# Kernel tuning notes

Hardware: AMD Instinct MI355X
Metric: run time of the kernel (lower is better)

## Reference

```python
import jax, jax.numpy as jnp
import numpy as np

H = 12        # num attention heads
W = 256       # one-sided window (attention_window // 2)
NEG = -1e9    # additive mask value


def setup_inputs() -> dict:
    key = jax.random.key(0)
    ks = jax.random.split(key, 6)
    B, S, D = 2, 4096, 768
    inp = {
        "hidden_states": jax.random.normal(ks[0], (B, S, D), dtype=jnp.float32),
        "attention_mask": jnp.zeros((B, S), dtype=jnp.float32),
        "Wq": jax.random.normal(ks[1], (D, D), dtype=jnp.float32) * 0.02,
        "bq": jnp.zeros((D,), dtype=jnp.float32),
        "Wk": jax.random.normal(ks[2], (D, D), dtype=jnp.float32) * 0.02,
        "bk": jnp.zeros((D,), dtype=jnp.float32),
        "Wv": jax.random.normal(ks[3], (D, D), dtype=jnp.float32) * 0.02,
        "bv": jnp.zeros((D,), dtype=jnp.float32),
        "Wo": jax.random.normal(ks[4], (D, D), dtype=jnp.float32) * 0.02,
        "bo": jnp.zeros((D,), dtype=jnp.float32),
    }
    return inp


def _sliding_window_attn(hidden_states, attention_mask, Wq, bq, Wk, bk, Wv, bv, Wo, bo):
    B, S, D = hidden_states.shape
    dh = D // H
    b = W                 # chunk size == one-sided window
    nb = S // b           # number of chunks (S must be multiple of W)

    # projections; Longformer scales the query by 1/sqrt(d_head)
    q = (hidden_states @ Wq.T + bq) / jnp.sqrt(jnp.float32(dh))
    k = hidden_states @ Wk.T + bk
    v = hidden_states @ Wv.T + bv

    # [B, H, S, dh]
    q = q.reshape(B, S, H, dh).transpose(0, 2, 1, 3)
    k = k.reshape(B, S, H, dh).transpose(0, 2, 1, 3)
    v = v.reshape(B, S, H, dh).transpose(0, 2, 1, 3)

    # chunk queries: [B, H, nb, b, dh]
    qb = q.reshape(B, H, nb, b, dh)

    # pad K/V by one chunk on each side, gather 3 consecutive chunks per query chunk
    kp = jnp.pad(k, ((0, 0), (0, 0), (b, b), (0, 0)))
    vp = jnp.pad(v, ((0, 0), (0, 0), (b, b), (0, 0)))
    idx = jnp.arange(nb)[:, None] * b + jnp.arange(3 * b)[None, :]  # [nb, 3b] into padded seq
    kw = kp[:, :, idx]  # [B, H, nb, 3b, dh]
    vw = vp[:, :, idx]  # [B, H, nb, 3b, dh]

    # banded scores: [B, H, nb, b, 3b]
    scores = jnp.einsum("bhnqd,bhnkd->bhnqk", qb, kw)

    # band mask: query at local pos qi (global n*b+qi) vs key at local pos ki
    # (global n*b + ki - b); relative offset = ki - b - qi, keep |offset| <= W
    rel = jnp.arange(3 * b)[None, :] - b - jnp.arange(b)[:, None]      # [b, 3b]
    band = jnp.abs(rel) <= W
    # sequence-boundary mask: key global position must lie in [0, S)
    kpos = idx - b                                                      # [nb, 3b]
    inbounds = (kpos >= 0) & (kpos < S)
    valid = band[None, :, :] & inbounds[:, None, :]                     # [nb, b, 3b]

    # key padding bias from attention_mask (wrapper passes attention_mask * -1)
    neg_mask = attention_mask * -1.0                                    # [B, S]
    mp = jnp.pad(neg_mask, ((0, 0), (b, b)))
    key_bias = mp[:, idx]                                               # [B, nb, 3b]

    scores = scores + key_bias[:, None, :, None, :]
    scores = jnp.where(valid[None, None], scores, NEG)

    probs = jax.nn.softmax(scores, axis=-1)
    ctx = jnp.einsum("bhnqk,bhnkd->bhnqd", probs, vw)                   # [B, H, nb, b, dh]
    ctx = ctx.reshape(B, H, S, dh).transpose(0, 2, 1, 3).reshape(B, S, D)

    return ctx @ Wo.T + bo


def reference(hidden_states, attention_mask, Wq, bq, Wk, bk, Wv, bv, Wo, bo):
    return _sliding_window_attn(hidden_states, attention_mask,
                                Wq, bq, Wk, bk, Wv, bv, Wo, bo)
```

## Files before the change

### kernel.cpp

```cpp
#include <hip/hip_runtime.h>
#include <hip/hip_bf16.h>
#include <stdint.h>

#define NH 12
#define DH 64
#define SEQ 4096
#define DM 768
#define NEGV -1e9f
#define LOG2E 1.4426950408889634f
#define QSCALE 0.1803368801111601f

using bf16x8 = __attribute__((ext_vector_type(8))) short;
using f32x4  = __attribute__((ext_vector_type(4))) float;

static __device__ __forceinline__ short f2bf(float f) {
  unsigned u = __builtin_bit_cast(unsigned, f);
  u += 0x7fffu + ((u >> 16) & 1u);
  return (short)(u >> 16);
}

static __device__ __forceinline__ unsigned pack2bf(float lo, float hi) {
  unsigned a = __builtin_bit_cast(unsigned, lo);
  a += 0x7fffu + ((a >> 16) & 1u);
  unsigned b = __builtin_bit_cast(unsigned, hi);
  b += 0x7fffu + ((b >> 16) & 1u);
  return (a >> 16) | (b & 0xffff0000u);
}

static __device__ __forceinline__ void gload16(const void* g, void* l) {
  __builtin_amdgcn_global_load_lds(
      (const __attribute__((address_space(1))) unsigned*)g,
      (__attribute__((address_space(3))) unsigned*)l, 16, 0, 0);
}

static __device__ __forceinline__ f32x4 mfma16(bf16x8 a, bf16x8 b, f32x4 c) {
  return __builtin_amdgcn_mfma_f32_16x16x32_bf16(a, b, c, 0, 0, 0);
}

#define SBAR() __builtin_amdgcn_sched_barrier(0)
#define WAIT8() asm volatile("s_waitcnt vmcnt(8)" ::: "memory")
#define WAIT4() asm volatile("s_waitcnt vmcnt(4)" ::: "memory")
#define WAIT0() asm volatile("s_waitcnt vmcnt(0)" ::: "memory")
#define LKWAIT() asm volatile("s_waitcnt lgkmcnt(0)" ::: "memory")
#define HBAR() __builtin_amdgcn_s_barrier()

__global__ __launch_bounds__(256) void cvt_x(const float* __restrict__ X,
                                             short* __restrict__ Xb, int n4) {
  int i = blockIdx.x * 256 + threadIdx.x;
  if (i >= n4) return;
  float4 v = ((const float4*)X)[i];
  short4 o; o.x = f2bf(v.x); o.y = f2bf(v.y); o.z = f2bf(v.z); o.w = f2bf(v.w);
  ((short4*)Xb)[i] = o;
}

__global__ __launch_bounds__(256) void cvt_w(
    const float* __restrict__ Wq, const float* __restrict__ Wk,
    const float* __restrict__ Wv, const float* __restrict__ Wo,
    short* __restrict__ Wqkv, short* __restrict__ Wob) {
  int i = blockIdx.x * 256 + threadIdx.x;
  const int n1 = 2304 * 768 / 4;
  if (i < n1) {
    int e = i * 4;
    int row = e / 768;
    const float* src;
    float sc = 1.0f;
    if (row < 768)       { src = Wq + e; sc = QSCALE; }
    else if (row < 1536) { src = Wk + e - 768 * 768; }
    else                 { src = Wv + e - 1536 * 768; }
    float4 v = *(const float4*)src;
    short4 o; o.x = f2bf(v.x * sc); o.y = f2bf(v.y * sc);
    o.z = f2bf(v.z * sc); o.w = f2bf(v.w * sc);
    ((short4*)Wqkv)[i] = o;
  } else {
    int j = i - n1;
    if (j >= 768 * 768 / 4) return;
    float4 v = ((const float4*)Wo)[j];
    short4 o; o.x = f2bf(v.x); o.y = f2bf(v.y); o.z = f2bf(v.z); o.w = f2bf(v.w);
    ((short4*)Wob)[j] = o;
  }
}

#define GEMM_PIPELINE(SM, AG, BG, ACC, LANE, WR, WC)                           \
  {                                                                            \
    const int l15 = (LANE) & 15, gw = (LANE) >> 4;                             \
    const int s_ = (l15 >> 1) & 3;                                             \
    const int fcol = ((gw ^ s_) << 3);                                         \
    const int NT = 24;                                             \
    auto stage = [&](int t) {                                                  \
      short* ab = (SM) + ((t & 3) << 12);                                      \
      short* bb = (SM) + 16384 + ((t & 3) << 12);                              \
      int kt = t << 5;                                                         \
      gload16((AG) + kt, ab + ldst);                                           \
      gload16((AG) + kt + 64 * 768, ab + ldst + 2048);                         \
      gload16((BG) + kt, bb + ldst);                                           \
      gload16((BG) + kt + 64 * 768, bb + ldst + 2048);                         \
    };                                                                         \
    auto compute = [&](int t) {                                                \
      const short* ab = (SM) + ((t & 3) << 12);                                \
      const short* bb = (SM) + 16384 + ((t & 3) << 12);                        \
      bf16x8 af[4], bf[4];                                                     \
      _Pragma("unroll") for (int mi = 0; mi < 4; ++mi)                         \
          af[mi] = *(const bf16x8*)(ab + ((WR) + mi * 16 + l15) * 32 + fcol);  \
      _Pragma("unroll") for (int ni = 0; ni < 4; ++ni)                         \
          bf[ni] = *(const bf16x8*)(bb + ((WC) + ni * 16 + l15) * 32 + fcol);  \
      __builtin_amdgcn_s_setprio(1);                                           \
      _Pragma("unroll") for (int mi = 0; mi < 4; ++mi)                         \
          _Pragma("unroll") for (int ni = 0; ni < 4; ++ni)                     \
              ACC[mi][ni] = mfma16(af[mi], bf[ni], ACC[mi][ni]);               \
      __builtin_amdgcn_s_setprio(0);                                           \
    };                                                                         \
    stage(0); stage(1); stage(2);                                              \
    SBAR();                                                                    \
    _Pragma("unroll 1") for (int i = 0; i < NT - 3; ++i) {                     \
      SBAR(); WAIT8(); HBAR(); SBAR();                                         \
      stage(i + 3);                                                            \
      SBAR();                                                                  \
      compute(i);                                                              \
    }                                                                          \
    SBAR(); WAIT8(); HBAR(); SBAR(); compute(NT - 3);                          \
    SBAR(); WAIT4(); HBAR(); SBAR(); compute(NT - 2);                          \
    SBAR(); WAIT0(); HBAR(); SBAR(); compute(NT - 1);                          \
  }

__global__ __launch_bounds__(256) void gemm_qkv(
    const short* __restrict__ Xb, const short* __restrict__ Wqkv,
    const float* __restrict__ bq, const float* __restrict__ bk,
    const float* __restrict__ bv,
    short* __restrict__ qO, short* __restrict__ kO, short* __restrict__ vT) {
  __shared__ __align__(16) short sm[32768];
  const int tid = threadIdx.x, lane = tid & 63, wid = tid >> 6;
  const int xcd = blockIdx.x & 7, kk = blockIdx.x >> 3;
  const int m0 = (xcd * 8 + (kk & 7)) * 128;
  const int n0 = (kk >> 3) * 128;
  const int wr = (wid >> 1) * 64, wc = (wid & 1) * 64;
  const int srow = tid >> 2;
  const int scol = (((tid & 3) ^ ((srow >> 1) & 3)) << 3);
  const short* Ag = Xb + (m0 + srow) * 768 + scol;
  const short* Bg = Wqkv + (n0 + srow) * 768 + scol;
  const int ldst = tid * 8;

  const int src = n0 / 768;
  const int nloc = n0 % 768;
  float bias[4];
#pragma unroll
  for (int ni = 0; ni < 4; ++ni) {
    int c = nloc + wc + ni * 16 + (lane & 15);
    bias[ni] = (src == 0) ? bq[c] * QSCALE : (src == 1) ? bk[c] : bv[c];
  }
  WAIT0(); SBAR();

  f32x4 acc[4][4] = {};
  GEMM_PIPELINE(sm, Ag, Bg, acc, lane, wr, wc);

  const int bb = m0 >> 12;
  const int s0 = m0 & (SEQ - 1);
  __syncthreads();
  if (src < 2) {
#pragma unroll
    for (int mi = 0; mi < 4; ++mi)
#pragma unroll
      for (int ni = 0; ni < 4; ++ni) {
        int row = wr + mi * 16 + ((lane >> 4) << 2);
        int col = wc + ni * 16 + (lane & 15);
#pragma unroll
        for (int r = 0; r < 4; ++r)
          sm[(row + r) * 132 + col] = f2bf(acc[mi][ni][r] + bias[ni]);
      }
    __syncthreads();
    short* dst = (src == 0) ? qO : kO;
    for (int u = tid; u < 8192; u += 256) {
      int r = u >> 6, cp = (u & 63) << 1;
      unsigned val = *(const unsigned*)&sm[r * 132 + cp];
      int c = nloc + cp;
      int h = c >> 6, d = c & 63;
      *(unsigned*)&dst[(((bb * NH + h) * SEQ) + s0 + r) * DH + d] = val;
    }
  } else {
#pragma unroll
    for (int mi = 0; mi < 4; ++mi)
#pragma unroll
      for (int ni = 0; ni < 4; ++ni) {
        int row = wr + mi * 16 + ((lane >> 4) << 2);
        int col = wc + ni * 16 + (lane & 15);
        short4 pk;
        pk.x = f2bf(acc[mi][ni][0] + bias[ni]);
        pk.y = f2bf(acc[mi][ni][1] + bias[ni]);
        pk.z = f2bf(acc[mi][ni][2] + bias[ni]);
        pk.w = f2bf(acc[mi][ni][3] + bias[ni]);
        *(short4*)&sm[col * 132 + row] = pk;
      }
    __syncthreads();
    for (int u = tid; u < 8192; u += 256) {
      int cc = u >> 6, rp = (u & 63) << 1;
      unsigned val = *(const unsigned*)&sm[cc * 132 + rp];
      int c = nloc + cc;
      int h = c >> 6, d = c & 63;
      *(unsigned*)&vT[(((bb * NH + h) * DH) + d) * SEQ + s0 + rp] = val;
    }
  }
}

__global__ __launch_bounds__(512, 4) void attn(
    const short* __restrict__ qI, const short* __restrict__ kI,
    const short* __restrict__ vT, const float* __restrict__ amask,
    short* __restrict__ ctx) {
  __shared__ __align__(16) short Ks[128 * 64];
  __shared__ __align__(16) short Vs[64 * 128];
  __shared__ __align__(16) short Ps[8][16 * 132];
  __shared__ __align__(16) float BiasL[768];
  const int tid = threadIdx.x, lane = tid & 63, wid = tid >> 6;
  const int vb_id = (blockIdx.x & 7) * 96 + (blockIdx.x >> 3);
  const int strip = vb_id & 31;
  const int hh = (vb_id >> 5) % 12;
  const int bb = vb_id / 384;
  const int s0 = strip * 128;
  const int n = s0 >> 8;
  const int i0 = s0 & 255;
  const int base = (n - 1) * 256;
  const int bh = bb * NH + hh;
  const int m = lane & 15, hq = lane >> 4;
  const int swz = m & 7;
  const int iw = i0 + (wid << 4);

  const short* qbase = qI + ((size_t)(bh * SEQ) + s0 + (wid << 4)) * DH;
  const bf16x8 aq0 = *(const bf16x8*)(qbase + m * DH + (hq << 3));
  const bf16x8 aq1 = *(const bf16x8*)(qbase + m * DH + 32 + (hq << 3));

  const int kb_s0 = m * 64 + ((hq ^ swz) << 3);
  const int kb_s1 = m * 64 + (((hq + 4) ^ swz) << 3);
  const int vk0 = m * 128 + ((hq ^ swz) << 3);
  const int vk1 = m * 128 + (((hq + 4) ^ swz) << 3);
  const int vk2 = m * 128 + (((hq + 8) ^ swz) << 3);
  const int vk3 = m * 128 + (((hq + 12) ^ swz) << 3);
  short* Pw = Ps[wid];
  const int pwr = m * 132;

  const int e0 = tid * 8, e1 = tid * 8 + 4096;
  const int kj0 = e0 >> 6, kj1 = e1 >> 6;
  const int ksrc0 = kj0 * DH + ((((e0 >> 3) & 7) ^ (kj0 & 7)) << 3);
  const int ksrc1 = kj1 * DH + ((((e1 >> 3) & 7) ^ (kj1 & 7)) << 3);
  const int vd0 = e0 >> 7, vd1 = e1 >> 7;
  const int vsrc0 = vd0 * SEQ + ((((e0 >> 3) & 15) ^ (vd0 & 7)) << 3);
  const int vsrc1 = vd1 * SEQ + ((((e1 >> 3) & 15) ^ (vd1 & 7)) << 3);

  const short* kg0 = kI + (size_t)bh * SEQ * DH;
  const short* vg0 = vT + (size_t)bh * DH * SEQ;

  if (tid < 192) {
    int idx = base + tid * 4;
    idx = idx < 0 ? 0 : (idx > SEQ - 4 ? SEQ - 4 : idx);
    float4 bv = *(const float4*)(amask + bb * SEQ + idx);
    *(float4*)&BiasL[tid * 4] = bv;
  }

  int cl0 = (n == 0) ? 2 : 0;
  if (i0 == 128 && cl0 < 1) cl0 = 1;
  int chi = (i0 == 0) ? 4 : 5;
  if (n == 15) chi = 3;

  uint4 rk0, rk1, rv0, rv1;
  {
    const int kpos0 = base + (cl0 << 7);
    const short* kb = kg0 + (size_t)kpos0 * DH;
    rk0 = *(const uint4*)(kb + ksrc0);
    rk1 = *(const uint4*)(kb + ksrc1);
    const short* vbp = vg0 + kpos0;
    rv0 = *(const uint4*)(vbp + vsrc0);
    rv1 = *(const uint4*)(vbp + vsrc1);
  }

  f32x4 acc[4] = {};
  float mrow = -1e30f, lrow = 0.f;

#pragma unroll 1
  for (int cc = cl0; cc <= chi; ++cc) {
    const int j0 = cc << 7;
    SBAR(); LKWAIT(); HBAR(); SBAR();
    *(uint4*)((short*)Ks + e0) = rk0;
    *(uint4*)((short*)Ks + e1) = rk1;
    *(uint4*)((short*)Vs + e0) = rv0;
    *(uint4*)((short*)Vs + e1) = rv1;
    SBAR(); LKWAIT(); HBAR(); SBAR();

    f32x4 sc[8];
    __builtin_amdgcn_s_setprio(1);
#pragma unroll
    for (int jt = 0; jt < 8; ++jt) {
      bf16x8 k0 = *(const bf16x8*)(Ks + jt * 1024 + kb_s0);
      bf16x8 k1 = *(const bf16x8*)(Ks + jt * 1024 + kb_s1);
      f32x4 z = {};
      z = mfma16(k0, aq0, z);
      z = mfma16(k1, aq1, z);
      sc[jt] = z;
    }
    __builtin_amdgcn_s_setprio(0);

    if (cc < chi) {
      const int kposn = base + ((cc + 1) << 7);
      const short* kb = kg0 + (size_t)kposn * DH;
      rk0 = *(const uint4*)(kb + ksrc0);
      rk1 = *(const uint4*)(kb + ksrc1);
      const short* vbp = vg0 + kposn;
      rv0 = *(const uint4*)(vbp + vsrc0);
      rv1 = *(const uint4*)(vbp + vsrc1);
    }

    float mn = mrow;
    const bool interior = (j0 >= iw + 15) && (j0 <= iw + 385);
    const float* bl = BiasL + j0 + (hq << 2);
    if (interior) {
#pragma unroll
      for (int jt = 0; jt < 8; ++jt) {
        float4 b4 = *(const float4*)(bl + jt * 16);
#pragma unroll
        for (int r = 0; r < 4; ++r) {
          float s = fmaf(-LOG2E, (&b4.x)[r], sc[jt][r]);
          sc[jt][r] = s;
          mn = fmaxf(mn, s);
        }
      }
    } else {
      const int iq = iw + m;
#pragma unroll
      for (int jt = 0; jt < 8; ++jt) {
        float4 b4 = *(const float4*)(bl + jt * 16);
        const int jb = j0 + jt * 16 + (hq << 2);
#pragma unroll
        for (int r = 0; r < 4; ++r) {
          int j = jb + r;
          float s = fmaf(-LOG2E, (&b4.x)[r], sc[jt][r]);
          s = (j >= iq && j <= iq + 512) ? s : NEGV;
          sc[jt][r] = s;
          mn = fmaxf(mn, s);
        }
      }
    }
    mn = fmaxf(mn, __shfl_xor(mn, 16));
    mn = fmaxf(mn, __shfl_xor(mn, 32));

    const bool resc = !__all(mn - mrow <= 4.0f);
    const float mbase = resc ? mn : mrow;

    float l0 = 0.f;
#pragma unroll
    for (int jt = 0; jt < 8; ++jt) {
      float p0 = exp2f(sc[jt][0] - mbase);
      float p1 = exp2f(sc[jt][1] - mbase);
      float p2 = exp2f(sc[jt][2] - mbase);
      float p3 = exp2f(sc[jt][3] - mbase);
      l0 += (p0 + p1) + (p2 + p3);
      uint2 u;
      u.x = pack2bf(p0, p1);
      u.y = pack2bf(p2, p3);
      *(uint2*)(Pw + pwr + jt * 16 + (hq << 2)) = u;
    }
    l0 += __shfl_xor(l0, 16);
    l0 += __shfl_xor(l0, 32);
    if (resc) {
      const float scl = exp2f(mrow - mn);
      lrow = lrow * scl + l0;
      mrow = mn;
      const float s0r = __shfl(scl, (hq << 2) + 0);
      const float s1r = __shfl(scl, (hq << 2) + 1);
      const float s2r = __shfl(scl, (hq << 2) + 2);
      const float s3r = __shfl(scl, (hq << 2) + 3);
#pragma unroll
      for (int nt = 0; nt < 4; ++nt) {
        acc[nt][0] *= s0r; acc[nt][1] *= s1r;
        acc[nt][2] *= s2r; acc[nt][3] *= s3r;
      }
    } else {
      lrow += l0;
    }

    LKWAIT(); SBAR();

    __builtin_amdgcn_s_setprio(1);
#pragma unroll
    for (int ks = 0; ks < 4; ++ks) {
      bf16x8 pa = *(const bf16x8*)(Pw + pwr + ks * 32 + (hq << 3));
      const int vkk = (ks == 0) ? vk0 : (ks == 1) ? vk1 : (ks == 2) ? vk2 : vk3;
#pragma unroll
      for (int nt = 0; nt < 4; ++nt) {
        bf16x8 vv = *(const bf16x8*)(Vs + nt * 2048 + vkk);
        acc[nt] = mfma16(pa, vv, acc[nt]);
      }
    }
    __builtin_amdgcn_s_setprio(0);
  }

  const float inv = 1.0f / lrow;
  const float i0r = __shfl(inv, (hq << 2) + 0);
  const float i1r = __shfl(inv, (hq << 2) + 1);
  const float i2r = __shfl(inv, (hq << 2) + 2);
  const float i3r = __shfl(inv, (hq << 2) + 3);
#pragma unroll
  for (int nt = 0; nt < 4; ++nt) {
    Pw[((hq << 2) + 0) * 72 + nt * 16 + m] = f2bf(acc[nt][0] * i0r);
    Pw[((hq << 2) + 1) * 72 + nt * 16 + m] = f2bf(acc[nt][1] * i1r);
    Pw[((hq << 2) + 2) * 72 + nt * 16 + m] = f2bf(acc[nt][2] * i2r);
    Pw[((hq << 2) + 3) * 72 + nt * 16 + m] = f2bf(acc[nt][3] * i3r);
  }
  LKWAIT(); SBAR();
#pragma unroll
  for (int it = 0; it < 2; ++it) {
    int row = it * 8 + (lane >> 3);
    bf16x8 val = *(const bf16x8*)(Pw + row * 72 + ((lane & 7) << 3));
    *(bf16x8*)(ctx + ((size_t)(bb * SEQ) + s0 + (wid << 4) + row) * DM +
               hh * DH + ((lane & 7) << 3)) = val;
  }
}

__global__ __launch_bounds__(256) void gemm_out(
    const short* __restrict__ Cb, const short* __restrict__ Wob,
    const float* __restrict__ bo, float* __restrict__ out) {
  __shared__ __align__(16) short sm[32768];
  const int tid = threadIdx.x, lane = tid & 63, wid = tid >> 6;
  const int xcd = blockIdx.x & 7, kk = blockIdx.x >> 3;
  const int m0 = (xcd * 8 + (kk & 7)) * 128;
  const int n0 = (kk >> 3) * 128;
  const int wr = (wid >> 1) * 64, wc = (wid & 1) * 64;
  const int srow = tid >> 2;
  const int scol = (((tid & 3) ^ ((srow >> 1) & 3)) << 3);
  const short* Ag = Cb + (m0 + srow) * 768 + scol;
  const short* Bg = Wob + (n0 + srow) * 768 + scol;
  const int ldst = tid * 8;

  float bias[4];
#pragma unroll
  for (int ni = 0; ni < 4; ++ni)
    bias[ni] = bo[n0 + wc + ni * 16 + (lane & 15)];
  WAIT0(); SBAR();

  f32x4 acc[4][4] = {};
  GEMM_PIPELINE(sm, Ag, Bg, acc, lane, wr, wc);

#pragma unroll
  for (int mi = 0; mi < 4; ++mi)
#pragma unroll
    for (int ni = 0; ni < 4; ++ni) {
      int row = m0 + wr + mi * 16 + ((lane >> 4) << 2);
      int col = n0 + wc + ni * 16 + (lane & 15);
#pragma unroll
      for (int r = 0; r < 4; ++r)
        out[(row + r) * DM + col] = acc[mi][ni][r] + bias[ni];
    }
}

extern "C" void kernel_launch(void* const* d_in, const int* in_sizes, int n_in,
                              void* d_out, int out_size, void* d_ws, size_t ws_size,
                              hipStream_t stream) {
  (void)in_sizes; (void)n_in; (void)out_size; (void)ws_size;
  const float* hs    = (const float*)d_in[0];
  const float* amask = (const float*)d_in[1];
  const float* Wq = (const float*)d_in[2];
  const float* bq = (const float*)d_in[3];
  const float* Wk = (const float*)d_in[4];
  const float* bk = (const float*)d_in[5];
  const float* Wv = (const float*)d_in[6];
  const float* bv = (const float*)d_in[7];
  const float* Wo = (const float*)d_in[8];
  const float* bo = (const float*)d_in[9];
  float* out = (float*)d_out;
  char* ws = (char*)d_ws;
  short* Xb   = (short*)(ws);
  short* Wqkv = (short*)(ws + 12582912);
  short* Wob  = (short*)(ws + 16121856);
  short* qB   = (short*)(ws + 17301504);
  short* kB   = (short*)(ws + 29884416);
  short* vTB  = (short*)(ws + 42467328);
  short* ctx  = Xb;

  cvt_x<<<dim3(6144), dim3(256), 0, stream>>>(hs, Xb, 8192 * 768 / 4);
  cvt_w<<<dim3(2304), dim3(256), 0, stream>>>(Wq, Wk, Wv, Wo, Wqkv, Wob);
  gemm_qkv<<<dim3(1152), dim3(256), 0, stream>>>(Xb, Wqkv, bq, bk, bv, qB, kB, vTB);
  attn<<<dim3(768), dim3(512), 0, stream>>>(qB, kB, vTB, amask, ctx);
  gemm_out<<<dim3(384), dim3(256), 0, stream>>>(ctx, Wob, bo, out);
}
```

Before: 145.0 us.

## Double-buffer K/V tiles in LDS with direct global-to-LDS async loads

Replaces the register-staged K/V prefetch (global→registers→LDS writes) with direct global-to-LDS loads into a double-buffered shared-memory ring. The next chunk is issued into the alternate buffer at the top of each iteration, so the load overlaps the QK and PV MFMA work. This drops the per-iteration register round-trip and LDS store phase and frees VGPRs. In exchange it doubles K/V LDS usage and removes the occupancy hint from launch_bounds, which may reduce blocks per CU.

```diff
diff --git a/kernel.cpp b/kernel.cpp
--- a/kernel.cpp
+++ b/kernel.cpp
@@ -200,12 +200,12 @@
   }
 }
 
-__global__ __launch_bounds__(512, 4) void attn(
+__global__ __launch_bounds__(512) void attn(
     const short* __restrict__ qI, const short* __restrict__ kI,
     const short* __restrict__ vT, const float* __restrict__ amask,
     short* __restrict__ ctx) {
-  __shared__ __align__(16) short Ks[128 * 64];
-  __shared__ __align__(16) short Vs[64 * 128];
+  __shared__ __align__(16) short Ks[2][8192];
+  __shared__ __align__(16) short Vs[2][8192];
   __shared__ __align__(16) short Ps[8][16 * 132];
   __shared__ __align__(16) float BiasL[768];
   const int tid = threadIdx.x, lane = tid & 63, wid = tid >> 6;
@@ -258,52 +258,43 @@
   int chi = (i0 == 0) ? 4 : 5;
   if (n == 15) chi = 3;
 
-  uint4 rk0, rk1, rv0, rv1;
-  {
-    const int kpos0 = base + (cl0 << 7);
+  auto stageKV = [&](int c, int buf) {
+    const int kpos0 = base + (c << 7);
     const short* kb = kg0 + (size_t)kpos0 * DH;
-    rk0 = *(const uint4*)(kb + ksrc0);
-    rk1 = *(const uint4*)(kb + ksrc1);
+    gload16(kb + ksrc0, (short*)Ks[buf] + e0);
+    gload16(kb + ksrc1, (short*)Ks[buf] + e1);
     const short* vbp = vg0 + kpos0;
-    rv0 = *(const uint4*)(vbp + vsrc0);
-    rv1 = *(const uint4*)(vbp + vsrc1);
-  }
+    gload16(vbp + vsrc0, (short*)Vs[buf] + e0);
+    gload16(vbp + vsrc1, (short*)Vs[buf] + e1);
+  };
+
+  stageKV(cl0, 0);
 
   f32x4 acc[4] = {};
   float mrow = -1e30f, lrow = 0.f;
+  int p = 0;
 
 #pragma unroll 1
   for (int cc = cl0; cc <= chi; ++cc) {
     const int j0 = cc << 7;
-    SBAR(); LKWAIT(); HBAR(); SBAR();
-    *(uint4*)((short*)Ks + e0) = rk0;
-    *(uint4*)((short*)Ks + e1) = rk1;
-    *(uint4*)((short*)Vs + e0) = rv0;
-    *(uint4*)((short*)Vs + e1) = rv1;
-    SBAR(); LKWAIT(); HBAR(); SBAR();
-
+    SBAR(); WAIT0(); HBAR(); SBAR();
+    if (cc < chi) stageKV(cc + 1, p ^ 1);
+    SBAR();
+
+    const short* Kp = Ks[p];
+    const short* Vp = Vs[p];
     f32x4 sc[8];
     __builtin_amdgcn_s_setprio(1);
 #pragma unroll
     for (int jt = 0; jt < 8; ++jt) {
-      bf16x8 k0 = *(const bf16x8*)(Ks + jt * 1024 + kb_s0);
-      bf16x8 k1 = *(const bf16x8*)(Ks + jt * 1024 + kb_s1);
+      bf16x8 k0 = *(const bf16x8*)(Kp + jt * 1024 + kb_s0);
+      bf16x8 k1 = *(const bf16x8*)(Kp + jt * 1024 + kb_s1);
       f32x4 z = {};
       z = mfma16(k0, aq0, z);
       z = mfma16(k1, aq1, z);
       sc[jt] = z;
     }
     __builtin_amdgcn_s_setprio(0);
-
-    if (cc < chi) {
-      const int kposn = base + ((cc + 1) << 7);
-      const short* kb = kg0 + (size_t)kposn * DH;
-      rk0 = *(const uint4*)(kb + ksrc0);
-      rk1 = *(const uint4*)(kb + ksrc1);
-      const short* vbp = vg0 + kposn;
-      rv0 = *(const uint4*)(vbp + vsrc0);
-      rv1 = *(const uint4*)(vbp + vsrc1);
-    }
 
     float mn = mrow;
     const bool interior = (j0 >= iw + 15) && (j0 <= iw + 385);
@@ -382,11 +373,12 @@
       const int vkk = (ks == 0) ? vk0 : (ks == 1) ? vk1 : (ks == 2) ? vk2 : vk3;
 #pragma unroll
       for (int nt = 0; nt < 4; ++nt) {
-        bf16x8 vv = *(const bf16x8*)(Vs + nt * 2048 + vkk);
+        bf16x8 vv = *(const bf16x8*)(Vp + nt * 2048 + vkk);
         acc[nt] = mfma16(pa, vv, acc[nt]);
       }
     }
     __builtin_amdgcn_s_setprio(0);
+    p ^= 1;
   }
 
   const float inv = 1.0f / lrow;
```

Result: faster. 135.9 us (-6.3%).

## Process two query tiles per wave in attention with 4-wave blocks and direct LDS loads

Applied to the files above, without the earlier changes.

The attention kernel now runs 4 waves per block, with each wave handling 32 query rows as two 16-row MFMA tiles. Each K and V fragment read from LDS therefore feeds twice as many MFMAs. The register-staged K/V prefetch is replaced by gload16 direct-to-LDS loads between plain barriers, which drops the overlap with compute. The softmax now uses per-lane partial maxima with a lazy rescale threshold of 8, defers the row-sum reduction to the end, and folds -log2e into the mask bias. Register pressure rises from the doubled accumulators, and removing the prefetch may expose load latency.

```diff
diff --git a/kernel.cpp b/kernel.cpp
--- a/kernel.cpp
+++ b/kernel.cpp
@@ -200,13 +200,13 @@
   }
 }
 
-__global__ __launch_bounds__(512, 4) void attn(
+__global__ __launch_bounds__(256) void attn(
     const short* __restrict__ qI, const short* __restrict__ kI,
     const short* __restrict__ vT, const float* __restrict__ amask,
     short* __restrict__ ctx) {
-  __shared__ __align__(16) short Ks[128 * 64];
-  __shared__ __align__(16) short Vs[64 * 128];
-  __shared__ __align__(16) short Ps[8][16 * 132];
+  __shared__ __align__(16) short Ks[8192];
+  __shared__ __align__(16) short Vs[8192];
+  __shared__ __align__(16) short Ps[4][32 * 132];
   __shared__ __align__(16) float BiasL[768];
   const int tid = threadIdx.x, lane = tid & 63, wid = tid >> 6;
   const int vb_id = (blockIdx.x & 7) * 96 + (blockIdx.x >> 3);
@@ -220,11 +220,13 @@
   const int bh = bb * NH + hh;
   const int m = lane & 15, hq = lane >> 4;
   const int swz = m & 7;
-  const int iw = i0 + (wid << 4);
-
-  const short* qbase = qI + ((size_t)(bh * SEQ) + s0 + (wid << 4)) * DH;
-  const bf16x8 aq0 = *(const bf16x8*)(qbase + m * DH + (hq << 3));
-  const bf16x8 aq1 = *(const bf16x8*)(qbase + m * DH + 32 + (hq << 3));
+  const int iw = i0 + (wid << 5);
+
+  const short* qbase = qI + ((size_t)(bh * SEQ) + s0 + (wid << 5)) * DH;
+  bf16x8 aq00 = *(const bf16x8*)(qbase + m * DH + (hq << 3));
+  bf16x8 aq01 = *(const bf16x8*)(qbase + m * DH + 32 + (hq << 3));
+  bf16x8 aq10 = *(const bf16x8*)(qbase + (16 + m) * DH + (hq << 3));
+  bf16x8 aq11 = *(const bf16x8*)(qbase + (16 + m) * DH + 32 + (hq << 3));
 
   const int kb_s0 = m * 64 + ((hq ^ swz) << 3);
   const int kb_s1 = m * 64 + (((hq + 4) ^ swz) << 3);
@@ -233,15 +235,18 @@
   const int vk2 = m * 128 + (((hq + 8) ^ swz) << 3);
   const int vk3 = m * 128 + (((hq + 12) ^ swz) << 3);
   short* Pw = Ps[wid];
-  const int pwr = m * 132;
-
-  const int e0 = tid * 8, e1 = tid * 8 + 4096;
-  const int kj0 = e0 >> 6, kj1 = e1 >> 6;
-  const int ksrc0 = kj0 * DH + ((((e0 >> 3) & 7) ^ (kj0 & 7)) << 3);
-  const int ksrc1 = kj1 * DH + ((((e1 >> 3) & 7) ^ (kj1 & 7)) << 3);
-  const int vd0 = e0 >> 7, vd1 = e1 >> 7;
-  const int vsrc0 = vd0 * SEQ + ((((e0 >> 3) & 15) ^ (vd0 & 7)) << 3);
-  const int vsrc1 = vd1 * SEQ + ((((e1 >> 3) & 15) ^ (vd1 & 7)) << 3);
+  const int pwr0 = m * 132;
+  const int pwr1 = (16 + m) * 132;
+
+  int ksrcA[1], dummy;
+  (void)dummy; (void)ksrcA;
+  const int eb = tid * 8;
+#define KSRC(p) ({ int e_ = (p)*2048 + eb; int kj_ = e_ >> 6;                 \
+                   kj_ * DH + ((((e_ >> 3) & 7) ^ (kj_ & 7)) << 3); })
+#define VSRC(p) ({ int e_ = (p)*2048 + eb; int vd_ = e_ >> 7;                 \
+                   vd_ * SEQ + ((((e_ >> 3) & 15) ^ (vd_ & 7)) << 3); })
+  const int ks0 = KSRC(0), ks1 = KSRC(1), ks2 = KSRC(2), ks3 = KSRC(3);
+  const int vs0 = VSRC(0), vs1 = VSRC(1), vs2 = VSRC(2), vs3 = VSRC(3);
 
   const short* kg0 = kI + (size_t)bh * SEQ * DH;
   const short* vg0 = vT + (size_t)bh * DH * SEQ;
@@ -250,6 +255,7 @@
     int idx = base + tid * 4;
     idx = idx < 0 ? 0 : (idx > SEQ - 4 ? SEQ - 4 : idx);
     float4 bv = *(const float4*)(amask + bb * SEQ + idx);
+    bv.x *= -LOG2E; bv.y *= -LOG2E; bv.z *= -LOG2E; bv.w *= -LOG2E;
     *(float4*)&BiasL[tid * 4] = bv;
   }
 
@@ -258,69 +264,62 @@
   int chi = (i0 == 0) ? 4 : 5;
   if (n == 15) chi = 3;
 
-  uint4 rk0, rk1, rv0, rv1;
-  {
-    const int kpos0 = base + (cl0 << 7);
-    const short* kb = kg0 + (size_t)kpos0 * DH;
-    rk0 = *(const uint4*)(kb + ksrc0);
-    rk1 = *(const uint4*)(kb + ksrc1);
-    const short* vbp = vg0 + kpos0;
-    rv0 = *(const uint4*)(vbp + vsrc0);
-    rv1 = *(const uint4*)(vbp + vsrc1);
-  }
-
-  f32x4 acc[4] = {};
-  float mrow = -1e30f, lrow = 0.f;
+  f32x4 acc0[4] = {}, acc1[4] = {};
+  float mrow0 = -1e30f, mrow1 = -1e30f, lrow0 = 0.f, lrow1 = 0.f;
 
 #pragma unroll 1
   for (int cc = cl0; cc <= chi; ++cc) {
     const int j0 = cc << 7;
-    SBAR(); LKWAIT(); HBAR(); SBAR();
-    *(uint4*)((short*)Ks + e0) = rk0;
-    *(uint4*)((short*)Ks + e1) = rk1;
-    *(uint4*)((short*)Vs + e0) = rv0;
-    *(uint4*)((short*)Vs + e1) = rv1;
-    SBAR(); LKWAIT(); HBAR(); SBAR();
-
-    f32x4 sc[8];
+    const int kpos0 = base + j0;
+    __syncthreads();
+    {
+      const short* kb = kg0 + (size_t)kpos0 * DH;
+      gload16(kb + ks0, Ks + eb);
+      gload16(kb + ks1, Ks + 2048 + eb);
+      gload16(kb + ks2, Ks + 4096 + eb);
+      gload16(kb + ks3, Ks + 6144 + eb);
+      const short* vbp = vg0 + kpos0;
+      gload16(vbp + vs0, Vs + eb);
+      gload16(vbp + vs1, Vs + 2048 + eb);
+      gload16(vbp + vs2, Vs + 4096 + eb);
+      gload16(vbp + vs3, Vs + 6144 + eb);
+    }
+    __syncthreads();
+
+    f32x4 sc0[8], sc1[8];
     __builtin_amdgcn_s_setprio(1);
 #pragma unroll
     for (int jt = 0; jt < 8; ++jt) {
       bf16x8 k0 = *(const bf16x8*)(Ks + jt * 1024 + kb_s0);
       bf16x8 k1 = *(const bf16x8*)(Ks + jt * 1024 + kb_s1);
-      f32x4 z = {};
-      z = mfma16(k0, aq0, z);
-      z = mfma16(k1, aq1, z);
-      sc[jt] = z;
+      f32x4 z0 = {}, z1 = {};
+      z0 = mfma16(k0, aq00, z0);
+      z0 = mfma16(k1, aq01, z0);
+      z1 = mfma16(k0, aq10, z1);
+      z1 = mfma16(k1, aq11, z1);
+      sc0[jt] = z0;
+      sc1[jt] = z1;
     }
     __builtin_amdgcn_s_setprio(0);
 
-    if (cc < chi) {
-      const int kposn = base + ((cc + 1) << 7);
-      const short* kb = kg0 + (size_t)kposn * DH;
-      rk0 = *(const uint4*)(kb + ksrc0);
-      rk1 = *(const uint4*)(kb + ksrc1);
-      const short* vbp = vg0 + kposn;
-      rv0 = *(const uint4*)(vbp + vsrc0);
-      rv1 = *(const uint4*)(vbp + vsrc1);
-    }
-
-    float mn = mrow;
-    const bool interior = (j0 >= iw + 15) && (j0 <= iw + 385);
+    const bool interior = (j0 >= iw + 31) && (j0 <= iw + 385);
     const float* bl = BiasL + j0 + (hq << 2);
+    float mp0[4] = {-3e38f, -3e38f, -3e38f, -3e38f};
+    float mp1[4] = {-3e38f, -3e38f, -3e38f, -3e38f};
     if (interior) {
 #pragma unroll
       for (int jt = 0; jt < 8; ++jt) {
         float4 b4 = *(const float4*)(bl + jt * 16);
 #pragma unroll
         for (int r = 0; r < 4; ++r) {
-          float s = fmaf(-LOG2E, (&b4.x)[r], sc[jt][r]);
-          sc[jt][r] = s;
-          mn = fmaxf(mn, s);
+          float s0v = sc0[jt][r] + (&b4.x)[r];
+          float s1v = sc1[jt][r] + (&b4.x)[r];
+          sc0[jt][r] = s0v; mp0[r] = fmaxf(mp0[r], s0v);
+          sc1[jt][r] = s1v; mp1[r] = fmaxf(mp1[r], s1v);
         }
       }
     } else {
-      const int iq = iw + m;
+      const int iq0 = iw + m, iq1 = iw + 16 + m;
 #pragma unroll
       for (int jt = 0; jt < 8; ++jt) {
         float4 b4 = *(const float4*)(bl + jt * 16);
@@ -328,49 +327,72 @@
 #pragma unroll
         for (int r = 0; r < 4; ++r) {
           int j = jb + r;
-          float s = fmaf(-LOG2E, (&b4.x)[r], sc[jt][r]);
-          s = (j >= iq && j <= iq + 512) ? s : NEGV;
-          sc[jt][r] = s;
-          mn = fmaxf(mn, s);
+          float s0v = sc0[jt][r] + (&b4.x)[r];
+          float s1v = sc1[jt][r] + (&b4.x)[r];
+          s0v = (j >= iq0 && j <= iq0 + 512) ? s0v : NEGV;
+          s1v = (j >= iq1 && j <= iq1 + 512) ? s1v : NEGV;
+          sc0[jt][r] = s0v; mp0[r] = fmaxf(mp0[r], s0v);
+          sc1[jt][r] = s1v; mp1[r] = fmaxf(mp1[r], s1v);
         }
       }
     }
-    mn = fmaxf(mn, __shfl_xor(mn, 16));
-    mn = fmaxf(mn, __shfl_xor(mn, 32));
-
-    const bool resc = !__all(mn - mrow <= 4.0f);
-    const float mbase = resc ? mn : mrow;
-
-    float l0 = 0.f;
+    const float mx0 = fmaxf(fmaxf(mp0[0], mp0[1]), fmaxf(mp0[2], mp0[3]));
+    const float mx1 = fmaxf(fmaxf(mp1[0], mp1[1]), fmaxf(mp1[2], mp1[3]));
+
+    const bool resc = __any((mx0 > mrow0 + 8.0f) | (mx1 > mrow1 + 8.0f));
+    float scl0 = 1.f, scl1 = 1.f;
+    if (resc) {
+      float mn0 = fmaxf(mrow0, mx0), mn1 = fmaxf(mrow1, mx1);
+      mn0 = fmaxf(mn0, __shfl_xor(mn0, 16));
+      mn0 = fmaxf(mn0, __shfl_xor(mn0, 32));
+      mn1 = fmaxf(mn1, __shfl_xor(mn1, 16));
+      mn1 = fmaxf(mn1, __shfl_xor(mn1, 32));
+      scl0 = exp2f(mrow0 - mn0);
+      scl1 = exp2f(mrow1 - mn1);
+      mrow0 = mn0; mrow1 = mn1;
+    }
+
+    float l0a = 0.f, l0b = 0.f;
 #pragma unroll
     for (int jt = 0; jt < 8; ++jt) {
-      float p0 = exp2f(sc[jt][0] - mbase);
-      float p1 = exp2f(sc[jt][1] - mbase);
-      float p2 = exp2f(sc[jt][2] - mbase);
-      float p3 = exp2f(sc[jt][3] - mbase);
-      l0 += (p0 + p1) + (p2 + p3);
+      float p0 = exp2f(sc0[jt][0] - mrow0);
+      float p1 = exp2f(sc0[jt][1] - mrow0);
+      float p2 = exp2f(sc0[jt][2] - mrow0);
+      float p3 = exp2f(sc0[jt][3] - mrow0);
+      l0a += (p0 + p1) + (p2 + p3);
       uint2 u;
       u.x = pack2bf(p0, p1);
       u.y = pack2bf(p2, p3);
-      *(uint2*)(Pw + pwr + jt * 16 + (hq << 2)) = u;
-    }
-    l0 += __shfl_xor(l0, 16);
-    l0 += __shfl_xor(l0, 32);
+      *(uint2*)(Pw + pwr0 + jt * 16 + (hq << 2)) = u;
+      float q0 = exp2f(sc1[jt][0] - mrow1);
+      float q1 = exp2f(sc1[jt][1] - mrow1);
+      float q2 = exp2f(sc1[jt][2] - mrow1);
+      float q3 = exp2f(sc1[jt][3] - mrow1);
+      l0b += (q0 + q1) + (q2 + q3);
+      uint2 w;
+      w.x = pack2bf(q0, q1);
+      w.y = pack2bf(q2, q3);
+      *(uint2*)(Pw + pwr1 + jt * 16 + (hq << 2)) = w;
+    }
     if (resc) {
-      const float scl = exp2f(mrow - mn);
-      lrow = lrow * scl + l0;
-      mrow = mn;
-      const float s0r = __shfl(scl, (hq << 2) + 0);
-      const float s1r = __shfl(scl, (hq << 2) + 1);
-      const float s2r = __shfl(scl, (hq << 2) + 2);
-      const float s3r = __shfl(scl, (hq << 2) + 3);
-#pragma unroll
-      for (int nt = 0; nt < 4; ++nt) {
-        acc[nt][0] *= s0r; acc[nt][1] *= s1r;
-        acc[nt][2] *= s2r; acc[nt][3] *= s3r;
+      lrow0 = lrow0 * scl0 + l0a;
+      lrow1 = lrow1 * scl1 + l0b;
+      float sa[4], sb[4];
+#pragma unroll
+      for (int r = 0; r < 4; ++r) {
+        sa[r] = __shfl(scl0, (hq << 2) + r);
+        sb[r] = __shfl(scl1, (hq << 2) + r);
       }
+#pragma unroll
+      for (int nt = 0; nt < 4; ++nt)
+#pragma unroll
+        for (int r = 0; r < 4; ++r) {
+          acc0[nt][r] *= sa[r];
+          acc1[nt][r] *= sb[r];
+        }
     } else {
-      lrow += l0;
+      lrow0 += l0a;
+      lrow1 += l0b;
     }
 
     LKWAIT(); SBAR();
@@ -378,35 +400,45 @@
     __builtin_amdgcn_s_setprio(1);
 #pragma unroll
     for (int ks = 0; ks < 4; ++ks) {
-      bf16x8 pa = *(const bf16x8*)(Pw + pwr + ks * 32 + (hq << 3));
       const int vkk = (ks == 0) ? vk0 : (ks == 1) ? vk1 : (ks == 2) ? vk2 : vk3;
+      bf16x8 pa0 = *(const bf16x8*)(Pw + pwr0 + ks * 32 + (hq << 3));
+      bf16x8 pa1 = *(const bf16x8*)(Pw + pwr1 + ks * 32 + (hq << 3));
 #pragma unroll
       for (int nt = 0; nt < 4; ++nt) {
         bf16x8 vv = *(const bf16x8*)(Vs + nt * 2048 + vkk);
-        acc[nt] = mfma16(pa, vv, acc[nt]);
+        acc0[nt] = mfma16(pa0, vv, acc0[nt]);
+        acc1[nt] = mfma16(pa1, vv, acc1[nt]);
       }
     }
     __builtin_amdgcn_s_setprio(0);
   }
 
-  const float inv = 1.0f / lrow;
-  const float i0r = __shfl(inv, (hq << 2) + 0);
-  const float i1r = __shfl(inv, (hq << 2) + 1);
-  const float i2r = __shfl(inv, (hq << 2) + 2);
-  const float i3r = __shfl(inv, (hq << 2) + 3);
-#pragma unroll
-  for (int nt = 0; nt < 4; ++nt) {
-    Pw[((hq << 2) + 0) * 72 + nt * 16 + m] = f2bf(acc[nt][0] * i0r);
-    Pw[((hq << 2) + 1) * 72 + nt * 16 + m] = f2bf(acc[nt][1] * i1r);
-    Pw[((hq << 2) + 2) * 72 + nt * 16 + m] = f2bf(acc[nt][2] * i2r);
-    Pw[((hq << 2) + 3) * 72 + nt * 16 + m] = f2bf(acc[nt][3] * i3r);
-  }
+  lrow0 += __shfl_xor(lrow0, 16);
+  lrow0 += __shfl_xor(lrow0, 32);
+  lrow1 += __shfl_xor(lrow1, 16);
+  lrow1 += __shfl_xor(lrow1, 32);
+  const float inv0 = 1.0f / lrow0;
+  const float inv1 = 1.0f / lrow1;
+  float ia[4], ib[4];
+#pragma unroll
+  for (int r = 0; r < 4; ++r) {
+    ia[r] = __shfl(inv0, (hq << 2) + r);
+    ib[r] = __shfl(inv1, (hq << 2) + r);
+  }
+  short* cw = Pw;
+#pragma unroll
+  for (int nt = 0; nt < 4; ++nt)
+#pragma unroll
+    for (int r = 0; r < 4; ++r) {
+      cw[((hq << 2) + r) * 72 + nt * 16 + m] = f2bf(acc0[nt][r] * ia[r]);
+      cw[(16 + (hq << 2) + r) * 72 + nt * 16 + m] = f2bf(acc1[nt][r] * ib[r]);
+    }
   LKWAIT(); SBAR();
 #pragma unroll
-  for (int it = 0; it < 2; ++it) {
+  for (int it = 0; it < 4; ++it) {
     int row = it * 8 + (lane >> 3);
-    bf16x8 val = *(const bf16x8*)(Pw + row * 72 + ((lane & 7) << 3));
-    *(bf16x8*)(ctx + ((size_t)(bb * SEQ) + s0 + (wid << 4) + row) * DM +
+    bf16x8 val = *(const bf16x8*)(cw + row * 72 + ((lane & 7) << 3));
+    *(bf16x8*)(ctx + ((size_t)(bb * SEQ) + s0 + (wid << 5) + row) * DM +
                hh * DH + ((lane & 7) << 3)) = val;
   }
 }
@@ -474,6 +506,6 @@
   cvt_x<<<dim3(6144), dim3(256), 0, stream>>>(hs, Xb, 8192 * 768 / 4);
   cvt_w<<<dim3(2304), dim3(256), 0, stream>>>(Wq, Wk, Wv, Wo, Wqkv, Wob);
   gemm_qkv<<<dim3(1152), dim3(256), 0, stream>>>(Xb, Wqkv, bq, bk, bv, qB, kB, vTB);
-  attn<<<dim3(768), dim3(512), 0, stream>>>(qB, kB, vTB, amask, ctx);
+  attn<<<dim3(768), dim3(256), 0, stream>>>(qB, kB, vTB, amask, ctx);
   gemm_out<<<dim3(384), dim3(256), 0, stream>>>(ctx, Wob, bo, out);
 }
```

Result: slower. 149.9 us (+3.4%).
